# Kernel tuning notes

Hardware: AMD Instinct MI355X
Metric: run time of the kernel (lower is better)

The kernel has to match this reference:

```python
import jax, jax.numpy as jnp
import numpy as np

FDIM = 512
H = W = 64
D_STATE = 16
D_INNER = 2 * FDIM
DT_RANK = FDIM // 16
K = 4


def conv2d(x, w, b=None, padding=0, dilation=1, groups=1):
    out = jax.lax.conv_general_dilated(
        x, w, (1, 1), [(padding, padding), (padding, padding)],
        rhs_dilation=(dilation, dilation), feature_group_count=groups,
        dimension_numbers=('NCHW', 'OIHW', 'NCHW'))
    if b is not None:
        out = out + b[None, :, None, None]
    return out


def layernorm(x, g, b, axes):
    mu = jnp.mean(x, axes, keepdims=True)
    var = jnp.var(x, axes, keepdims=True)
    return (x - mu) * jax.lax.rsqrt(var + 1e-5) * g + b


def channel_shuffle(x, groups):
    B, C, Hh, Ww = x.shape
    return x.reshape(B, groups, C // groups, Hh, Ww).transpose(0, 2, 1, 3, 4).reshape(B, C, Hh, Ww)


def selective_scan(u, delta, A, Bs, Cs, D):
    # u, delta: (B,K,d,L); A: (K,d,N); Bs, Cs: (B,K,N,L); D: (K,d)
    Bsz, Kk, d, L = u.shape
    N = A.shape[-1]
    dT = jnp.moveaxis(delta, -1, 0)  # (L,B,K,d)
    uT = jnp.moveaxis(u, -1, 0)
    BT = jnp.moveaxis(Bs, -1, 0)     # (L,B,K,N)
    CT = jnp.moveaxis(Cs, -1, 0)

    @jax.checkpoint
    def step(hprev, inp):
        dt, ut, bt, ct = inp
        dA = jnp.exp(dt[..., None] * A)                       # (B,K,d,N)
        hnew = dA * hprev + (dt * ut)[..., None] * bt[:, :, None, :]
        yt = jnp.einsum('bkdn,bkn->bkd', hnew, ct)
        return hnew, yt

    h0 = jnp.zeros((Bsz, Kk, d, N), u.dtype)
    _, ys = jax.lax.scan(step, h0, (dT, uT, BT, CT))          # ys: (L,B,K,d)
    y = jnp.moveaxis(ys, 0, -1)                               # (B,K,d,L)
    return y + D[None, :, :, None] * u


def ss2d_core(x, x_proj_w, dt_w, dt_b, A_logs, Ds):
    # x: (B, d_inner, H, W) -> y: (B, d_inner, L), VMamba 4-direction cross-scan
    B, d, Hh, Ww = x.shape
    L = Hh * Ww
    xf = x.reshape(B, d, L)
    xwh = jnp.swapaxes(x, 2, 3).reshape(B, d, L)
    x_hwwh = jnp.stack([xf, xwh], axis=1)                     # (B,2,d,L)
    xs = jnp.concatenate([x_hwwh, jnp.flip(x_hwwh, axis=-1)], axis=1)  # (B,4,d,L)
    x_dbl = jnp.einsum('bkdl,kcd->bkcl', xs, x_proj_w)
    dts, Bs, Cs = jnp.split(x_dbl, [DT_RANK, DT_RANK + D_STATE], axis=2)
    dts = jnp.einsum('bkrl,kdr->bkdl', dts, dt_w)
    delta = jax.nn.softplus(dts + dt_b[None, :, :, None])
    A = -jnp.exp(A_logs)
    out_y = selective_scan(xs, delta, A, Bs, Cs, Ds)          # (B,4,d,L)
    inv_y = jnp.flip(out_y[:, 2:4], axis=-1)
    wh_y = jnp.swapaxes(out_y[:, 1].reshape(B, d, Ww, Hh), 2, 3).reshape(B, d, L)
    invwh_y = jnp.swapaxes(inv_y[:, 1].reshape(B, d, Ww, Hh), 2, 3).reshape(B, d, L)
    return out_y[:, 0] + inv_y[:, 0] + wh_y + invwh_y


def setup_inputs() -> dict:
    key = jax.random.key(0)
    ks = jax.random.split(key, 16)
    rn = lambda k, shape, s=0.02: jax.random.normal(k, shape, jnp.float32) * s
    inp = {
        'feature_embedding': jax.random.normal(ks[0], (1, FDIM, H, W), jnp.float32),
        'latent_embedding': jax.random.normal(ks[1], (1, FDIM, H, W), jnp.float32),
        'fg_w1': rn(ks[2], (FDIM // 16, 2 * FDIM, 1, 1)),
        'fg_b1': jnp.zeros((FDIM // 16,), jnp.float32),
        'fg_w2': rn(ks[3], (2 * FDIM, FDIM // 16, 1, 1)),
        'fg_b2': jnp.zeros((2 * FDIM,), jnp.float32),
        'fb_w1': rn(ks[4], (FDIM, 2 * FDIM, 3, 3)),
        'ln_g': jnp.ones((FDIM, H, W), jnp.float32),
        'ln_b': jnp.zeros((FDIM, H, W), jnp.float32),
        'fb_dw_w': rn(ks[5], (FDIM, 1, 3, 3), 0.1),
        'fb_dw_b': jnp.zeros((FDIM,), jnp.float32),
        'fb_pw1_w': rn(ks[6], (FDIM, FDIM, 1, 1)),
        'fb_pw1_b': jnp.zeros((FDIM,), jnp.float32),
        'fb_pw2_w': rn(ks[7], (FDIM, FDIM, 1, 1)),
        'fb_pw2_b': jnp.zeros((FDIM,), jnp.float32),
        'ln1_g': jnp.ones((FDIM,), jnp.float32),
        'ln1_b': jnp.zeros((FDIM,), jnp.float32),
        'in_proj_w': rn(ks[8], (2 * D_INNER, FDIM)),
        'dconv_w': rn(ks[9], (D_INNER, 1, 3, 3), 0.1),
        'dconv_b': jnp.zeros((D_INNER,), jnp.float32),
        'x_proj_w': rn(ks[10], (K, DT_RANK + 2 * D_STATE, D_INNER)),
        'dt_w': rn(ks[11], (K, D_INNER, DT_RANK), 0.1),
        'dt_b': rn(ks[12], (K, D_INNER), 0.1) - 4.0,
        'A_logs': jnp.broadcast_to(jnp.log(jnp.arange(1, D_STATE + 1, dtype=jnp.float32)), (K, D_INNER, D_STATE)) + 0.0,
        'Ds': jnp.ones((K, D_INNER), jnp.float32),
        'out_norm_g': jnp.ones((D_INNER,), jnp.float32),
        'out_norm_b': jnp.zeros((D_INNER,), jnp.float32),
        'out_proj_w': rn(ks[13], (FDIM, D_INNER)),
    }
    return inp


def reference(feature_embedding, latent_embedding, fg_w1, fg_b1, fg_w2, fg_b2,
              fb_w1, ln_g, ln_b, fb_dw_w, fb_dw_b, fb_pw1_w, fb_pw1_b,
              fb_pw2_w, fb_pw2_b, ln1_g, ln1_b, in_proj_w, dconv_w, dconv_b,
              x_proj_w, dt_w, dt_b, A_logs, Ds, out_norm_g, out_norm_b, out_proj_w):
    gelu = lambda v: jax.nn.gelu(v, approximate=False)
    concat = jnp.concatenate([feature_embedding, latent_embedding], axis=1)
    g = gelu(conv2d(concat, fg_w1, fg_b1))
    g = jax.nn.sigmoid(conv2d(g, fg_w2, fg_b2))
    wf = concat * g
    h = conv2d(wf, fb_w1, padding=1)
    h = gelu(layernorm(h, ln_g, ln_b, (1, 2, 3)))
    h = conv2d(h, fb_dw_w, fb_dw_b, padding=2, dilation=2, groups=FDIM)
    h = gelu(conv2d(h, fb_pw1_w, fb_pw1_b))
    h = channel_shuffle(h, 8)
    h = conv2d(h, fb_pw2_w, fb_pw2_b)
    fused = h + feature_embedding                              # (B,C,H,W)
    B = fused.shape[0]
    # VSSBlock: LN -> SS2D -> residual, operating on (B,H,W,C)
    x = jnp.transpose(fused, (0, 2, 3, 1))
    xn = layernorm(x, ln1_g, ln1_b, (3,))
    xz = xn @ in_proj_w.T                                      # (B,H,W,2*d_inner)
    xp, z = jnp.split(xz, 2, axis=-1)
    xc = jnp.transpose(xp, (0, 3, 1, 2))                       # (B,d_inner,H,W)
    xc = jax.nn.silu(conv2d(xc, dconv_w, dconv_b, padding=1, groups=D_INNER))
    y = ss2d_core(xc, x_proj_w, dt_w, dt_b, A_logs, Ds)        # (B,d_inner,L)
    y = jnp.transpose(y.reshape(B, D_INNER, H, W), (0, 2, 3, 1))
    y = layernorm(y, out_norm_g, out_norm_b, (3,))
    y = y * jax.nn.silu(z)
    attn = x + (y @ out_proj_w.T)                              # VSSBlock residual
    attn_out = jnp.transpose(attn, (0, 3, 1, 2))               # (B,C,H,W)
    blur_k = jnp.full((FDIM, 1, 3, 3), 1.0 / 9.0, attn_out.dtype)  # AvgPool2d(3,1,1)
    return conv2d(attn_out, blur_k, padding=1, groups=FDIM) + fused
```

## Files before the change

kernel.cpp:

```cpp
#include <hip/hip_runtime.h>


#define NT 4096
#define NCH 32
#define CHL 128

__device__ __forceinline__ float geluf(float x){ return 0.5f*x*(1.f+erff(x*0.70710678118654752f)); }
__device__ __forceinline__ float sigmf(float x){ return 1.f/(1.f+__expf(-x)); }
__device__ __forceinline__ float softplusf(float x){ return (x>20.f)? x : __logf(1.f+__expf(x)); }
__device__ __forceinline__ unsigned short f2b(float f){
  unsigned u = __float_as_uint(f);
  u += 0x7FFFu + ((u>>16)&1u);
  return (unsigned short)(u>>16);
}

template<int BMODE, int EPI, bool TRANSW, int ZB=0>
__launch_bounds__(256)
__global__ void k_gemm(int M, int K, int lda, int ldb,
    const float* __restrict__ A, const float* __restrict__ bias,
    const float* __restrict__ Bf, const float* __restrict__ Bc0,
    const float* __restrict__ Bc1, int rev, int shuf,
    const float* __restrict__ resf, float* __restrict__ out)
{
  __shared__ float smem[4352];
  float* As = smem;
  float* Bs = smem + 2176;
  const int t  = threadIdx.x;
  const int n0 = blockIdx.x*64, m0 = blockIdx.y*64;
  if (ZB==1){
    int z = blockIdx.z;
    A   += (size_t)z*64*1024;
    if (z&1) Bf = Bc0;
    rev  = (z>=2);
    out += (size_t)z*NT*64;
  } else if (ZB==2){
    int z = blockIdx.z;
    A    += (size_t)z*1024*32;
    bias += (size_t)z*1024;
    Bf   += (size_t)z*NT*64;
    out  += (size_t)z*1024*NT;
  }
  float acc[4][4] = {};

  for (int k0=0; k0<K; k0+=32){
    __syncthreads();
    {
      int m = t>>2, kk0 = (t&3)*8;
      float av[8] = {0,0,0,0,0,0,0,0};
      if (m0+m < M){
        const float* pa = A + (size_t)(m0+m)*lda + k0 + kk0;
        float4 a0 = *(const float4*)pa; float4 a1 = *(const float4*)(pa+4);
        av[0]=a0.x; av[1]=a0.y; av[2]=a0.z; av[3]=a0.w;
        av[4]=a1.x; av[5]=a1.y; av[6]=a1.z; av[7]=a1.w;
      }
      #pragma unroll
      for (int j=0;j<8;j++) As[(kk0+j)*68 + m] = av[j];
    }
    if (BMODE==2){
      int n = t>>2, kk0 = (t&3)*8;
      const float* p = Bf + (size_t)(n0+n)*ldb + k0 + kk0;
      float4 x0 = *(const float4*)p; float4 x1 = *(const float4*)(p+4);
      Bs[(kk0+0)*68+n]=x0.x; Bs[(kk0+1)*68+n]=x0.y; Bs[(kk0+2)*68+n]=x0.z; Bs[(kk0+3)*68+n]=x0.w;
      Bs[(kk0+4)*68+n]=x1.x; Bs[(kk0+5)*68+n]=x1.y; Bs[(kk0+6)*68+n]=x1.z; Bs[(kk0+7)*68+n]=x1.w;
    } else {
      int kk = t>>3, n8 = (t&7)*8;
      float bv[8];
      if (BMODE==0){
        int r = k0+kk; if (shuf) r = (r&7)*64 + (r>>3);
        const float* p = Bf + (size_t)r*NT;
        if (!rev){
          float4 x0 = *(const float4*)(p + n0+n8); float4 x1 = *(const float4*)(p + n0+n8+4);
          bv[0]=x0.x;bv[1]=x0.y;bv[2]=x0.z;bv[3]=x0.w;bv[4]=x1.x;bv[5]=x1.y;bv[6]=x1.z;bv[7]=x1.w;
        } else {
          const float* q = p + (4088 - n0 - n8);
          float4 x0 = *(const float4*)q; float4 x1 = *(const float4*)(q+4);
          bv[0]=x1.w;bv[1]=x1.z;bv[2]=x1.y;bv[3]=x1.x;bv[4]=x0.w;bv[5]=x0.z;bv[6]=x0.y;bv[7]=x0.x;
        }
      } else if (BMODE==1){
        int c = k0+kk;
        const float* p = (c<512) ? (Bc0 + (size_t)c*NT) : (Bc1 + (size_t)(c-512)*NT);
        float4 x0 = *(const float4*)(p + n0+n8); float4 x1 = *(const float4*)(p + n0+n8+4);
        bv[0]=x0.x;bv[1]=x0.y;bv[2]=x0.z;bv[3]=x0.w;bv[4]=x1.x;bv[5]=x1.y;bv[6]=x1.z;bv[7]=x1.w;
      } else {
        #pragma unroll
        for (int j=0;j<8;j++) bv[j] = 0.f;
      }
      *(float4*)&Bs[kk*68 + n8]   = make_float4(bv[0],bv[1],bv[2],bv[3]);
      *(float4*)&Bs[kk*68 + n8+4] = make_float4(bv[4],bv[5],bv[6],bv[7]);
    }
    __syncthreads();
    int ti = t>>4, tj = t&15;
    #pragma unroll
    for (int kk=0; kk<32; kk++){
      float4 a4 = *(const float4*)&As[kk*68 + ti*4];
      float4 b4 = *(const float4*)&Bs[kk*68 + tj*4];
      float aa[4] = {a4.x,a4.y,a4.z,a4.w};
      float bb[4] = {b4.x,b4.y,b4.z,b4.w};
      #pragma unroll
      for (int i=0;i<4;i++)
        #pragma unroll
        for (int j=0;j<4;j++) acc[i][j] += aa[i]*bb[j];
    }
  }

  int ti = t>>4, tj = t&15;
  if (!TRANSW){
    #pragma unroll
    for (int i=0;i<4;i++){
      int m = m0 + ti*4 + i;
      if (m >= M) continue;
      float bi = bias ? bias[m] : 0.f;
      float o4[4];
      #pragma unroll
      for (int j=0;j<4;j++){
        int n = n0 + tj*4 + j;
        float v = acc[i][j] + bi;
        if (EPI==1) v = geluf(v);
        else if (EPI==2) v = softplusf(v);
        else if (EPI==4) v = v + resf[(size_t)m*NT + n];
        else if (EPI==5){
          float cv = (m<512)? Bc0[(size_t)m*NT+n] : Bc1[(size_t)(m-512)*NT+n];
          v = cv * sigmf(v);
        }
        o4[j] = v;
      }
      *(float4*)&out[(size_t)m*NT + n0 + tj*4] = make_float4(o4[0],o4[1],o4[2],o4[3]);
    }
  } else {
    __syncthreads();
    #pragma unroll
    for (int i=0;i<4;i++)
      #pragma unroll
      for (int j=0;j<4;j++)
        smem[(tj*4+j)*68 + (ti*4+i)] = acc[i][j];
    __syncthreads();
    int nl = t>>2, c0 = (t&3)*16;
    #pragma unroll
    for (int g4=0; g4<4; g4++){
      float4 v = *(const float4*)&smem[nl*68 + c0 + g4*4];
      *(float4*)&out[(size_t)(n0+nl)*64 + c0 + g4*4] = v;
    }
  }
}

__global__ void k_cvt_bf16(const float* __restrict__ in, unsigned short* __restrict__ outp){
  size_t i = ((size_t)blockIdx.x*256 + threadIdx.x)*8;
  float4 a = *(const float4*)(in+i), b = *(const float4*)(in+i+4);
  unsigned short o[8] = { f2b(a.x),f2b(a.y),f2b(a.z),f2b(a.w),
                          f2b(b.x),f2b(b.y),f2b(b.z),f2b(b.w) };
  *(int4*)(outp+i) = *(int4*)o;
}

__global__ void k_cvt_wfrag(const float* __restrict__ w, int lda, int KSn,
                            unsigned short* __restrict__ outp){
  int tid = blockIdx.x*256 + threadIdx.x;
  int lane = tid & 63;
  int tmp = tid >> 6;
  int KS = tmp % KSn, MT = tmp / KSn;
  int m = MT*16 + (lane&15);
  int k = KS*32 + (lane>>4)*8;
  const float* p = w + (size_t)m*lda + k;
  float4 a = *(const float4*)p, b = *(const float4*)(p+4);
  unsigned short o[8] = { f2b(a.x),f2b(a.y),f2b(a.z),f2b(a.w),
                          f2b(b.x),f2b(b.y),f2b(b.z),f2b(b.w) };
  *(int4*)(outp + (size_t)tid*8) = *(int4*)o;
}

typedef __attribute__((ext_vector_type(8))) short bf16x8;
typedef __attribute__((ext_vector_type(4))) float f32x4;

__launch_bounds__(256)
__global__ void k_conv_mfma(const unsigned short* __restrict__ Wf,
                            const unsigned short* __restrict__ Bb,
                            float* __restrict__ outp){
  __shared__ unsigned short Bs[128*40];
  int t = threadIdx.x;
  int n0 = blockIdx.x*128, m0y = blockIdx.y;
  int kz = blockIdx.z;
  int w = t>>6, lane = t&63;
  int wm = (w>>1)*64, wn = (w&1)*64;
  int ln15 = lane&15, lhi = lane>>4;
  f32x4 acc[4][4] = {};
  int sn = t & 127, kh = t>>7;
  int p = n0 + sn, py = p>>6, px = p&63;

  for (int ks=0; ks<36; ks++){
    unsigned short tmp[16];
    int kbase = kz*1152 + ks*32 + kh*16;
    #pragma unroll
    for (int j=0;j<16;j++){
      int ka = kbase + j;
      int c = ka/9; int t9 = ka - c*9; int qy = t9/3;
      int dy = qy-1, dx = t9 - qy*3 - 1;
      int yy = py+dy, xx = px+dx;
      tmp[j] = (yy>=0 && yy<64 && xx>=0 && xx<64) ? Bb[(size_t)c*4096 + yy*64 + xx]
                                                  : (unsigned short)0;
    }
    __syncthreads();
    *(int4*)&Bs[sn*40 + kh*16]     = *(int4*)&tmp[0];
    *(int4*)&Bs[sn*40 + kh*16 + 8] = *(int4*)&tmp[8];
    __syncthreads();
    bf16x8 af[4], bf[4];
    int KSab = kz*36 + ks;
    #pragma unroll
    for (int fm=0; fm<4; fm++){
      int MT = m0y*8 + (w>>1)*4 + fm;
      af[fm] = *(const bf16x8*)&Wf[((size_t)MT*288 + KSab)*512 + lane*8];
    }
    #pragma unroll
    for (int fn=0; fn<4; fn++)
      bf[fn] = *(const bf16x8*)&Bs[(wn + fn*16 + ln15)*40 + lhi*8];
    #pragma unroll
    for (int fm=0; fm<4; fm++)
      #pragma unroll
      for (int fn=0; fn<4; fn++)
        acc[fm][fn] = __builtin_amdgcn_mfma_f32_16x16x32_bf16(af[fm], bf[fn], acc[fm][fn], 0,0,0);
  }
  float* op = outp + (size_t)kz*512*4096;
  #pragma unroll
  for (int fm=0; fm<4; fm++){
    #pragma unroll
    for (int fn=0; fn<4; fn++){
      int col = n0 + wn + fn*16 + ln15;
      int rowb = m0y*128 + wm + fm*16 + lhi*4;
      #pragma unroll
      for (int r=0; r<4; r++)
        op[(size_t)(rowb+r)*4096 + col] = acc[fm][fn][r];
    }
  }
}

template<int KSTEPS, int EPI>
__launch_bounds__(256)
__global__ void k_nhwc_mfma(const unsigned short* __restrict__ Wf,
                            const unsigned short* __restrict__ Bb, int ldb,
                            const float* __restrict__ resf,
                            float* __restrict__ outp){
  __shared__ unsigned short Bs[128*40];
  int t = threadIdx.x;
  int n0 = blockIdx.x*128, m0y = blockIdx.y;
  int w = t>>6, lane = t&63;
  int wm = (w>>1)*64, wn = (w&1)*64;
  int ln15 = lane&15, lhi = lane>>4;
  f32x4 acc[4][4] = {};
  int sn = t & 127, kh = t>>7;

  for (int ks=0; ks<KSTEPS; ks++){
    const unsigned short* src = Bb + (size_t)(n0+sn)*ldb + ks*32 + kh*16;
    int4 v0 = *(const int4*)src;
    int4 v1 = *(const int4*)(src+8);
    __syncthreads();
    *(int4*)&Bs[sn*40 + kh*16]     = v0;
    *(int4*)&Bs[sn*40 + kh*16 + 8] = v1;
    __syncthreads();
    bf16x8 af[4], bf[4];
    #pragma unroll
    for (int fm=0; fm<4; fm++){
      int MT = m0y*8 + (w>>1)*4 + fm;
      af[fm] = *(const bf16x8*)&Wf[((size_t)MT*KSTEPS + ks)*512 + lane*8];
    }
    #pragma unroll
    for (int fn=0; fn<4; fn++)
      bf[fn] = *(const bf16x8*)&Bs[(wn + fn*16 + ln15)*40 + lhi*8];
    #pragma unroll
    for (int fm=0; fm<4; fm++)
      #pragma unroll
      for (int fn=0; fn<4; fn++)
        acc[fm][fn] = __builtin_amdgcn_mfma_f32_16x16x32_bf16(af[fm], bf[fn], acc[fm][fn], 0,0,0);
  }
  #pragma unroll
  for (int fm=0; fm<4; fm++){
    #pragma unroll
    for (int fn=0; fn<4; fn++){
      int col = n0 + wn + fn*16 + ln15;
      int rowb = m0y*128 + wm + fm*16 + lhi*4;
      #pragma unroll
      for (int r=0; r<4; r++){
        float v = acc[fm][fn][r];
        if (EPI==4) v += resf[(size_t)(rowb+r)*4096 + col];
        outp[(size_t)(rowb+r)*4096 + col] = v;
      }
    }
  }
}

template<int DIL, int ACT>
__global__ void k_dwconv(const float* __restrict__ in, const float* __restrict__ w,
                         const float* __restrict__ b, float* __restrict__ out){
  int bid = blockIdx.x;
  int c = bid >> 4, yb = bid & 15;
  int t = threadIdx.x;
  int y = yb*4 + (t>>6), x = t&63;
  const float* pin = in + (size_t)c*NT;
  float acc = b[c];
  #pragma unroll
  for (int ky=0; ky<3; ky++){
    int yy = y + DIL*(ky-1);
    if (yy<0 || yy>=64) continue;
    #pragma unroll
    for (int kx=0; kx<3; kx++){
      int xx = x + DIL*(kx-1);
      if (xx<0 || xx>=64) continue;
      acc += w[c*9 + ky*3 + kx] * pin[yy*64+xx];
    }
  }
  if (ACT==1) acc = acc * sigmf(acc);
  out[(size_t)c*NT + y*64 + x] = acc;
}

__global__ void k_red_part8(const float* __restrict__ hp, float* __restrict__ h,
                            float* __restrict__ part){
  __shared__ float ls[256], lq[256];
  int t = threadIdx.x; size_t base = (size_t)blockIdx.x*4096 + t;
  const size_t SL = (size_t)512*4096;
  float s=0, q=0;
  #pragma unroll
  for (int i=0;i<16;i++){
    size_t idx = base + i*256;
    float v = 0.f;
    #pragma unroll
    for (int z=0; z<8; z++) v += hp[idx + z*SL];
    h[idx] = v; s+=v; q+=v*v;
  }
  ls[t]=s; lq[t]=q; __syncthreads();
  for (int off=128; off; off>>=1){ if (t<off){ ls[t]+=ls[t+off]; lq[t]+=lq[t+off]; } __syncthreads(); }
  if (t==0){ part[blockIdx.x] = ls[0]; part[512 + blockIdx.x] = lq[0]; }
}
__global__ void k_red_fin(const float* __restrict__ part, float* __restrict__ stats){
  __shared__ float ls[256], lq[256];
  int t = threadIdx.x;
  ls[t] = part[t] + part[t+256];
  lq[t] = part[512+t] + part[768+t];
  __syncthreads();
  for (int off=128; off; off>>=1){ if (t<off){ ls[t]+=ls[t+off]; lq[t]+=lq[t+off]; } __syncthreads(); }
  if (t==0){
    float mu = ls[0] * (1.f/2097152.f);
    float var = lq[0]*(1.f/2097152.f) - mu*mu;
    stats[0]=mu; stats[1]=rsqrtf(var + 1e-5f);
  }
}
__global__ void k_ln_gelu(const float* __restrict__ h, const float* __restrict__ g,
                          const float* __restrict__ b, const float* __restrict__ stats,
                          float* __restrict__ out){
  size_t idx = ((size_t)blockIdx.x*256 + threadIdx.x)*4;
  float mu = stats[0], rs = stats[1];
  float4 hv = *(const float4*)(h + idx);
  float4 gv = *(const float4*)(g + idx);
  float4 bv = *(const float4*)(b + idx);
  float4 o;
  o.x = geluf((hv.x-mu)*rs*gv.x+bv.x);
  o.y = geluf((hv.y-mu)*rs*gv.y+bv.y);
  o.z = geluf((hv.z-mu)*rs*gv.z+bv.z);
  o.w = geluf((hv.w-mu)*rs*gv.w+bv.w);
  *(float4*)(out + idx) = o;
}

__global__ void k_ln1_stats(const float* __restrict__ fused, float* __restrict__ mu1,
                            float* __restrict__ rs1){
  __shared__ float ss[256], sq[256];
  int t = threadIdx.x; int ci = t>>6; int pj = t&63;
  int pos = blockIdx.x*64 + pj;
  float s=0,q=0;
  for (int c=ci; c<512; c+=4){ float v = fused[(size_t)c*NT + pos]; s+=v; q+=v*v; }
  ss[t]=s; sq[t]=q; __syncthreads();
  if (ci==0){
    float S = ss[pj]+ss[64+pj]+ss[128+pj]+ss[192+pj];
    float Q = sq[pj]+sq[64+pj]+sq[128+pj]+sq[192+pj];
    float mu = S*(1.f/512.f);
    mu1[pos]=mu; rs1[pos]=rsqrtf(Q*(1.f/512.f) - mu*mu + 1e-5f);
  }
}
__global__ void k_ln1_apply(const float* __restrict__ fused, const float* __restrict__ g,
                            const float* __restrict__ b, const float* __restrict__ mu1,
                            const float* __restrict__ rs1, unsigned short* __restrict__ xnb){
  __shared__ float tile[64*65];
  int t = threadIdx.x;
  int p0 = blockIdx.x*64, c0 = blockIdx.y*64;
  for (int it=0; it<16; it++){
    int idx = t + it*256; int yy = idx>>6, xx = idx&63;
    tile[yy*65+xx] = fused[(size_t)(c0+yy)*NT + p0+xx];
  }
  __syncthreads();
  for (int it=0; it<16; it++){
    int idx = t + it*256; int r = idx>>6, s = idx&63;
    float v = tile[s*65+r];
    int pos = p0+r, c = c0+s;
    xnb[(size_t)pos*512 + c] = f2b((v - mu1[pos])*rs1[pos]*g[c] + b[c]);
  }
}

__global__ void k_transpose64(const float* __restrict__ in, float* __restrict__ out){
  __shared__ float tile[64*65];
  int d = blockIdx.x; int t = threadIdx.x;
  const float* p = in + (size_t)d*NT; float* q = out + (size_t)d*NT;
  for (int it=0; it<16; it++){
    int idx = t+it*256; int yy = idx>>6, xx = idx&63;
    tile[yy*65+xx] = p[idx];
  }
  __syncthreads();
  for (int it=0; it<16; it++){
    int idx = t+it*256; int w = idx>>6, hh = idx&63;
    q[idx] = tile[hh*65+w];
  }
}

__global__ void k_zero(float* __restrict__ p){
  size_t i = ((size_t)blockIdx.x*256 + threadIdx.x)*4;
  *(float4*)(p+i) = make_float4(0,0,0,0);
}

__launch_bounds__(256)
__global__ void k_scan_part(const float* __restrict__ delta, const float* __restrict__ xc,
                            const float* __restrict__ xcT, const float* __restrict__ xdblT,
                            const float* __restrict__ A_logs,
                            float* __restrict__ Pbuf, float* __restrict__ Sbuf){
  int bid = blockIdx.x;
  int c    = bid % NCH;
  int rest = bid / NCH;
  int k    = rest >> 4;
  int dblk = rest & 15;
  int w    = threadIdx.x >> 6;
  int lane = threadIdx.x & 63;
  int dsub = lane & 15, ngrp = lane >> 4;
  int d = dblk*64 + w*16 + dsub;
  const float* up = ((k&1)? xcT : xc) + (size_t)d*NT;
  const float* dp = delta + ((size_t)(k*1024 + d))*NT;
  const float* bc = xdblT + (size_t)k*NT*64;
  float A[4], S[4]={0,0,0,0}, P[4]={1.f,1.f,1.f,1.f};
  #pragma unroll
  for (int j=0;j<4;j++) A[j] = -__expf(A_logs[(size_t)(k*1024+d)*16 + ngrp*4 + j]);
  const bool rv = (k>=2);
  int base = c*CHL;
  for (int l0=base; l0<base+CHL; l0+=4){
    float4 dv4 = *(const float4*)(dp + l0);
    float4 uraw = rv ? *(const float4*)(up + (4092-l0)) : *(const float4*)(up + l0);
    float dts[4] = {dv4.x,dv4.y,dv4.z,dv4.w};
    float us[4];
    if (rv){ us[0]=uraw.w; us[1]=uraw.z; us[2]=uraw.y; us[3]=uraw.x; }
    else   { us[0]=uraw.x; us[1]=uraw.y; us[2]=uraw.z; us[3]=uraw.w; }
    #pragma unroll
    for (int s=0;s<4;s++){
      int l = l0+s;
      float dt = dts[s];
      float4 B4 = *(const float4*)(bc + (size_t)l*64 + 32 + ngrp*4);
      float xbu = dt*us[s];
      float Bv[4]={B4.x,B4.y,B4.z,B4.w};
      #pragma unroll
      for (int j=0;j<4;j++){
        float dA = __expf(dt*A[j]);
        S[j] = dA*S[j] + xbu*Bv[j];
        P[j] *= dA;
      }
    }
  }
  size_t o = ((size_t)(k*1024+d)*NCH + c)*16 + ngrp*4;
  *(float4*)&Pbuf[o] = make_float4(P[0],P[1],P[2],P[3]);
  *(float4*)&Sbuf[o] = make_float4(S[0],S[1],S[2],S[3]);
}

__global__ void k_scan_comb(const float* __restrict__ Pbuf, const float* __restrict__ Sbuf,
                            float* __restrict__ Hbuf){
  int tid = blockIdx.x*256 + threadIdx.x;
  int scan = tid >> 4, n = tid & 15;
  size_t base = (size_t)scan*(NCH*16) + n;
  float h = 0.f;
  #pragma unroll
  for (int c=0;c<NCH;c++){
    Hbuf[base + c*16] = h;
    h = Pbuf[base + c*16]*h + Sbuf[base + c*16];
  }
}

__launch_bounds__(256)
__global__ void k_scan_fin(const float* __restrict__ delta, const float* __restrict__ xc,
                           const float* __restrict__ xcT, const float* __restrict__ xdblT,
                           const float* __restrict__ A_logs, const float* __restrict__ Ds,
                           const float* __restrict__ Hbuf, float* __restrict__ ycomb){
  int bid = blockIdx.x;
  int c    = bid % NCH;
  int rest = bid / NCH;
  int k    = rest >> 4;
  int dblk = rest & 15;
  int w    = threadIdx.x >> 6;
  int lane = threadIdx.x & 63;
  int dsub = lane & 15, ngrp = lane >> 4;
  int d = dblk*64 + w*16 + dsub;
  const float* up = ((k&1)? xcT : xc) + (size_t)d*NT;
  const float* dp = delta + ((size_t)(k*1024 + d))*NT;
  const float* bc = xdblT + (size_t)k*NT*64;
  float A[4], h[4];
  #pragma unroll
  for (int j=0;j<4;j++) A[j] = -__expf(A_logs[(size_t)(k*1024+d)*16 + ngrp*4 + j]);
  {
    size_t o = ((size_t)(k*1024+d)*NCH + c)*16 + ngrp*4;
    float4 h4 = *(const float4*)&Hbuf[o];
    h[0]=h4.x; h[1]=h4.y; h[2]=h4.z; h[3]=h4.w;
  }
  float Dv = Ds[k*1024+d];
  const bool rv = (k>=2);
  int base = c*CHL;
  for (int l0=base; l0<base+CHL; l0+=4){
    float4 dv4 = *(const float4*)(dp + l0);
    float4 uraw = rv ? *(const float4*)(up + (4092-l0)) : *(const float4*)(up + l0);
    float dts[4] = {dv4.x,dv4.y,dv4.z,dv4.w};
    float us[4];
    if (rv){ us[0]=uraw.w; us[1]=uraw.z; us[2]=uraw.y; us[3]=uraw.x; }
    else   { us[0]=uraw.x; us[1]=uraw.y; us[2]=uraw.z; us[3]=uraw.w; }
    #pragma unroll
    for (int s=0;s<4;s++){
      int l = l0+s;
      float dt = dts[s], u = us[s];
      float4 B4 = *(const float4*)(bc + (size_t)l*64 + 32 + ngrp*4);
      float4 C4 = *(const float4*)(bc + (size_t)l*64 + 48 + ngrp*4);
      float xbu = dt*u;
      float Bv[4]={B4.x,B4.y,B4.z,B4.w}, Cv[4]={C4.x,C4.y,C4.z,C4.w};
      float ys = 0.f;
      #pragma unroll
      for (int j=0;j<4;j++){
        float dA = __expf(dt*A[j]);
        h[j] = dA*h[j] + xbu*Bv[j];
        ys += h[j]*Cv[j];
      }
      ys += __shfl_xor(ys, 16);
      ys += __shfl_xor(ys, 32);
      if (ngrp==0){
        int pos;
        if (k==0) pos = l;
        else if (k==1) pos = ((l&63)<<6) | (l>>6);
        else if (k==2) pos = 4095-l;
        else { int tt = 4095-l; pos = ((tt&63)<<6) | (tt>>6); }
        atomicAdd(&ycomb[(size_t)pos*1024 + d], ys + Dv*u);
      }
    }
  }
}

__global__ void k_combine(const float* __restrict__ ycomb, const float* __restrict__ xz,
                          const float* __restrict__ g, const float* __restrict__ b,
                          unsigned short* __restrict__ yactb){
  int pos = blockIdx.x, t = threadIdx.x;
  float v[4]; float s=0,q=0;
  #pragma unroll
  for (int i=0;i<4;i++){ v[i] = ycomb[(size_t)pos*1024 + t + i*256]; s+=v[i]; q+=v[i]*v[i]; }
  #pragma unroll
  for (int off=32; off>=1; off>>=1){ s += __shfl_xor(s,off); q += __shfl_xor(q,off); }
  __shared__ float red[8];
  int wid = t>>6;
  if ((t&63)==0){ red[wid*2]=s; red[wid*2+1]=q; }
  __syncthreads();
  float S = red[0]+red[2]+red[4]+red[6];
  float Q = red[1]+red[3]+red[5]+red[7];
  float mu = S*(1.f/1024.f), rs = rsqrtf(Q*(1.f/1024.f) - mu*mu + 1e-5f);
  #pragma unroll
  for (int i=0;i<4;i++){
    int dd = t + i*256;
    float z = xz[(size_t)(1024+dd)*NT + pos];
    float yv = (v[i]-mu)*rs*g[dd] + b[dd];
    yactb[(size_t)pos*1024 + dd] = f2b(yv * (z * sigmf(z)));
  }
}

__global__ void k_blur(const float* __restrict__ attn, const float* __restrict__ fused,
                       float* __restrict__ outp){
  int bid = blockIdx.x; int c = bid>>4, yb = bid&15; int t = threadIdx.x;
  int y = yb*4 + (t>>6), x = t&63;
  const float* p = attn + (size_t)c*NT;
  float s = 0;
  #pragma unroll
  for (int dy=-1; dy<=1; dy++){
    int yy = y+dy; if (yy<0||yy>=64) continue;
    #pragma unroll
    for (int dx=-1; dx<=1; dx++){
      int xx = x+dx; if (xx<0||xx>=64) continue;
      s += p[yy*64+xx];
    }
  }
  float val = s*(1.f/9.f) + fused[(size_t)c*NT + y*64 + x];
  outp[(size_t)c*NT + y*64 + x] = val;
}

extern "C" void kernel_launch(void* const* d_in, const int* in_sizes, int n_in,
                              void* d_out, int out_size, void* d_ws, size_t ws_size,
                              hipStream_t stream){
  const float* feat = (const float*)d_in[0];
  const float* lat  = (const float*)d_in[1];
  const float* fg_w1= (const float*)d_in[2];
  const float* fg_b1= (const float*)d_in[3];
  const float* fg_w2= (const float*)d_in[4];
  const float* fg_b2= (const float*)d_in[5];
  const float* fb_w1= (const float*)d_in[6];
  const float* ln_g = (const float*)d_in[7];
  const float* ln_b = (const float*)d_in[8];
  const float* dw_w = (const float*)d_in[9];
  const float* dw_b = (const float*)d_in[10];
  const float* pw1_w= (const float*)d_in[11];
  const float* pw1_b= (const float*)d_in[12];
  const float* pw2_w= (const float*)d_in[13];
  const float* pw2_b= (const float*)d_in[14];
  const float* ln1_g= (const float*)d_in[15];
  const float* ln1_b= (const float*)d_in[16];
  const float* inpw = (const float*)d_in[17];
  const float* dc_w = (const float*)d_in[18];
  const float* dc_b = (const float*)d_in[19];
  const float* xpw  = (const float*)d_in[20];
  const float* dtw  = (const float*)d_in[21];
  const float* dtb  = (const float*)d_in[22];
  const float* Alog = (const float*)d_in[23];
  const float* Dsp  = (const float*)d_in[24];
  const float* ong  = (const float*)d_in[25];
  const float* onb  = (const float*)d_in[26];
  const float* opw  = (const float*)d_in[27];
  float* outp = (float*)d_out;
  (void)in_sizes; (void)n_in; (void)out_size; (void)ws_size;

  float* Wp = (float*)d_ws;
  size_t off = 0;
  auto alloc = [&](size_t n){ float* p = Wp + off; off += n; return p; };
  float* S0    = alloc((size_t)1024*NT);
  float* S1    = alloc((size_t)512*NT);
  float* P0    = alloc((size_t)512*NT);
  float* P1    = alloc((size_t)2048*NT);
  float* P2    = alloc((size_t)1024*NT);
  float* P3    = alloc((size_t)1024*NT);
  float* P4    = alloc((size_t)4*NT*64);
  float* P5    = alloc((size_t)4*1024*NT);
  float* P6    = alloc((size_t)1024*NT);
  float* part  = alloc(1024);
  float* stats = alloc(4);
  float* mu1   = alloc(4096);
  float* rs1   = alloc(4096);

  float* wf    = S0;
  float* h     = S1;
  float* h2    = P1;
  float* h3    = S1;
  float* h4    = P2;
  float* fused = P0;
  float* xz    = P1;
  float* xc    = P2;
  float* xcT   = P3;
  float* xdblT = P4;
  float* hpart = P5;
  float* delta = P5;
  float* g1    = P6;
  float* ycomb = P6;
  float* attn  = S1;
  unsigned short* wf_bf   = (unsigned short*)(P1 + (size_t)512*NT);
  unsigned short* w_frag  = (unsigned short*)(P1 + (size_t)1024*NT);
  unsigned short* xnb     = (unsigned short*)S0;
  unsigned short* w_frag2 = (unsigned short*)P5;
  unsigned short* yactb   = (unsigned short*)S0;
  unsigned short* w_frag3 = (unsigned short*)P5;
  float* Pbuf  = S0;
  float* Sbuf  = S0 + (size_t)2*1048576;
  float* Hbuf  = S1;

  hipLaunchKernelGGL((k_gemm<1,1,false>), dim3(64,1), dim3(256), 0, stream,
      32, 1024, 1024, 0, fg_w1, fg_b1, nullptr, feat, lat, 0,0, nullptr, g1);
  hipLaunchKernelGGL((k_gemm<0,5,false>), dim3(64,16), dim3(256), 0, stream,
      1024, 32, 32, 0, fg_w2, fg_b2, g1, feat, lat, 0,0, nullptr, wf);
  hipLaunchKernelGGL(k_cvt_bf16, dim3(2048), dim3(256), 0, stream, wf, wf_bf);
  hipLaunchKernelGGL(k_cvt_wfrag, dim3(2304), dim3(256), 0, stream, fb_w1, 9216, 288, w_frag);
  hipLaunchKernelGGL(k_conv_mfma, dim3(32,4,8), dim3(256), 0, stream, w_frag, wf_bf, hpart);
  hipLaunchKernelGGL(k_red_part8, dim3(512), dim3(256), 0, stream, hpart, h, part);
  hipLaunchKernelGGL(k_red_fin,  dim3(1),   dim3(256), 0, stream, part, stats);
  hipLaunchKernelGGL(k_ln_gelu,  dim3(2048),dim3(256), 0, stream, h, ln_g, ln_b, stats, h2);
  hipLaunchKernelGGL((k_dwconv<2,0>), dim3(512*16), dim3(256), 0, stream, h2, dw_w, dw_b, h3);
  hipLaunchKernelGGL((k_gemm<0,1,false>), dim3(64,8), dim3(256), 0, stream,
      512, 512, 512, 0, pw1_w, pw1_b, h3, nullptr,nullptr, 0,0, nullptr, h4);
  hipLaunchKernelGGL((k_gemm<0,4,false>), dim3(64,8), dim3(256), 0, stream,
      512, 512, 512, 0, pw2_w, pw2_b, h4, nullptr,nullptr, 0,1, feat, fused);
  hipLaunchKernelGGL(k_ln1_stats, dim3(64), dim3(256), 0, stream, fused, mu1, rs1);
  hipLaunchKernelGGL(k_ln1_apply, dim3(64,8), dim3(256), 0, stream, fused, ln1_g, ln1_b, mu1, rs1, xnb);
  hipLaunchKernelGGL(k_cvt_wfrag, dim3(512), dim3(256), 0, stream, inpw, 512, 16, w_frag2);
  hipLaunchKernelGGL((k_nhwc_mfma<16,0>), dim3(32,16), dim3(256), 0, stream,
      w_frag2, xnb, 512, nullptr, xz);
  hipLaunchKernelGGL((k_dwconv<1,1>), dim3(1024*16), dim3(256), 0, stream, xz, dc_w, dc_b, xc);
  hipLaunchKernelGGL(k_transpose64, dim3(1024), dim3(256), 0, stream, xc, xcT);
  hipLaunchKernelGGL((k_gemm<0,0,true,1>), dim3(64,1,4), dim3(256), 0, stream,
      64, 1024, 1024, 0, xpw, nullptr, xc, xcT, nullptr, 0,0, nullptr, xdblT);
  hipLaunchKernelGGL((k_gemm<2,2,false,2>), dim3(64,16,4), dim3(256), 0, stream,
      1024, 32, 32, 64, dtw, dtb, xdblT, nullptr,nullptr, 0,0, nullptr, delta);
  hipLaunchKernelGGL(k_zero, dim3(4096), dim3(256), 0, stream, ycomb);
  hipLaunchKernelGGL(k_scan_part, dim3(64*NCH), dim3(256), 0, stream,
      delta, xc, xcT, xdblT, Alog, Pbuf, Sbuf);
  hipLaunchKernelGGL(k_scan_comb, dim3(256), dim3(256), 0, stream, Pbuf, Sbuf, Hbuf);
  hipLaunchKernelGGL(k_scan_fin, dim3(64*NCH), dim3(256), 0, stream,
      delta, xc, xcT, xdblT, Alog, Dsp, Hbuf, ycomb);
  hipLaunchKernelGGL(k_combine, dim3(4096), dim3(256), 0, stream, ycomb, xz, ong, onb, yactb);
  hipLaunchKernelGGL(k_cvt_wfrag, dim3(256), dim3(256), 0, stream, opw, 1024, 32, w_frag3);
  hipLaunchKernelGGL((k_nhwc_mfma<32,4>), dim3(32,4), dim3(256), 0, stream,
      w_frag3, yactb, 1024, fused, attn);
  hipLaunchKernelGGL(k_blur, dim3(512*16), dim3(256), 0, stream, attn, fused, outp);
}
```

Before: 1.052 ms.

## Move pointwise convs to bf16 MFMA GEMM and stage scan inputs in LDS

The two 512x512 pointwise convolutions in the feature block now run on the bf16 MFMA NHWC GEMM kernel instead of the fp32 generic GEMM. A new transpose-and-convert kernel produces bf16 NHWC activations, and the channel shuffle is folded into its index mapping. The MFMA kernel gains bias and GELU epilogues. Separately, both selective-scan kernels stage delta and u for 32-step chunks in shared memory with coalesced loads, replacing the per-thread strided row reads. The cost is extra conversion passes and lower precision in the pointwise convolutions.

```diff
diff --git a/kernel.cpp b/kernel.cpp
--- a/kernel.cpp
+++ b/kernel.cpp
@@ -151,6 +151,23 @@
   *(int4*)(outp+i) = *(int4*)o;
 }
 
+__global__ void k_cvtT_bf16(const float* __restrict__ in, int shuf,
+                            unsigned short* __restrict__ outp){
+  __shared__ float tile[64*65];
+  int t = threadIdx.x;
+  int p0 = blockIdx.x*64, c0 = blockIdx.y*64;
+  for (int it=0; it<16; it++){
+    int idx = t + it*256; int yy = idx>>6, xx = idx&63;
+    int c = c0 + yy; int src = shuf ? (c&7)*64 + (c>>3) : c;
+    tile[yy*65+xx] = in[(size_t)src*NT + p0+xx];
+  }
+  __syncthreads();
+  for (int it=0; it<16; it++){
+    int idx = t + it*256; int r = idx>>6, s = idx&63;
+    outp[(size_t)(p0+r)*512 + c0+s] = f2b(tile[s*65+r]);
+  }
+}
+
 __global__ void k_cvt_wfrag(const float* __restrict__ w, int lda, int KSn,
                             unsigned short* __restrict__ outp){
   int tid = blockIdx.x*256 + threadIdx.x;
@@ -234,6 +251,7 @@
 __launch_bounds__(256)
 __global__ void k_nhwc_mfma(const unsigned short* __restrict__ Wf,
                             const unsigned short* __restrict__ Bb, int ldb,
+                            const float* __restrict__ bias,
                             const float* __restrict__ resf,
                             float* __restrict__ outp){
   __shared__ unsigned short Bs[128*40];
@@ -276,9 +294,11 @@
       int rowb = m0y*128 + wm + fm*16 + lhi*4;
       #pragma unroll
       for (int r=0; r<4; r++){
-        float v = acc[fm][fn][r];
-        if (EPI==4) v += resf[(size_t)(rowb+r)*4096 + col];
-        outp[(size_t)(rowb+r)*4096 + col] = v;
+        int m = rowb + r;
+        float v = acc[fm][fn][r] + (bias ? bias[m] : 0.f);
+        if (EPI==1) v = geluf(v);
+        else if (EPI==4) v += resf[(size_t)m*4096 + col];
+        outp[(size_t)m*4096 + col] = v;
       }
     }
   }
@@ -414,36 +434,47 @@
                             const float* __restrict__ xcT, const float* __restrict__ xdblT,
                             const float* __restrict__ A_logs,
                             float* __restrict__ Pbuf, float* __restrict__ Sbuf){
+  __shared__ float dtile[64*36], utile[64*36];
   int bid = blockIdx.x;
   int c    = bid % NCH;
   int rest = bid / NCH;
   int k    = rest >> 4;
   int dblk = rest & 15;
-  int w    = threadIdx.x >> 6;
-  int lane = threadIdx.x & 63;
+  int t = threadIdx.x;
+  int w = t>>6, lane = t&63;
   int dsub = lane & 15, ngrp = lane >> 4;
-  int d = dblk*64 + w*16 + dsub;
-  const float* up = ((k&1)? xcT : xc) + (size_t)d*NT;
-  const float* dp = delta + ((size_t)(k*1024 + d))*NT;
+  int dd = w*16 + dsub;
+  int d = dblk*64 + dd;
+  int ld_dd = t>>2, q = t&3;
+  const bool rv = (k>=2);
+  const float* dprow = delta + ((size_t)(k*1024 + dblk*64 + ld_dd))*NT;
+  const float* uprow = ((k&1)? xcT : xc) + (size_t)(dblk*64 + ld_dd)*NT;
   const float* bc = xdblT + (size_t)k*NT*64;
   float A[4], S[4]={0,0,0,0}, P[4]={1.f,1.f,1.f,1.f};
   #pragma unroll
   for (int j=0;j<4;j++) A[j] = -__expf(A_logs[(size_t)(k*1024+d)*16 + ngrp*4 + j]);
-  const bool rv = (k>=2);
   int base = c*CHL;
-  for (int l0=base; l0<base+CHL; l0+=4){
-    float4 dv4 = *(const float4*)(dp + l0);
-    float4 uraw = rv ? *(const float4*)(up + (4092-l0)) : *(const float4*)(up + l0);
-    float dts[4] = {dv4.x,dv4.y,dv4.z,dv4.w};
-    float us[4];
-    if (rv){ us[0]=uraw.w; us[1]=uraw.z; us[2]=uraw.y; us[3]=uraw.x; }
-    else   { us[0]=uraw.x; us[1]=uraw.y; us[2]=uraw.z; us[3]=uraw.w; }
-    #pragma unroll
-    for (int s=0;s<4;s++){
-      int l = l0+s;
-      float dt = dts[s];
+  for (int l0=0; l0<CHL; l0+=32){
+    int L0 = base + l0;
+    __syncthreads();
+    {
+      const float* dp8 = dprow + L0 + q*8;
+      float4 a0 = *(const float4*)dp8, a1 = *(const float4*)(dp8+4);
+      *(float4*)&dtile[ld_dd*36 + q*8]     = a0;
+      *(float4*)&dtile[ld_dd*36 + q*8 + 4] = a1;
+      int us = rv ? (4064 - L0) : L0;
+      const float* up8 = uprow + us + q*8;
+      float4 b0 = *(const float4*)up8, b1 = *(const float4*)(up8+4);
+      *(float4*)&utile[ld_dd*36 + q*8]     = b0;
+      *(float4*)&utile[ld_dd*36 + q*8 + 4] = b1;
+    }
+    __syncthreads();
+    for (int s=0; s<32; s++){
+      int l = L0 + s;
+      float dt = dtile[dd*36 + s];
+      float u  = utile[dd*36 + (rv ? 31-s : s)];
       float4 B4 = *(const float4*)(bc + (size_t)l*64 + 32 + ngrp*4);
-      float xbu = dt*us[s];
+      float xbu = dt*u;
       float Bv[4]={B4.x,B4.y,B4.z,B4.w};
       #pragma unroll
       for (int j=0;j<4;j++){
@@ -476,17 +507,21 @@
                            const float* __restrict__ xcT, const float* __restrict__ xdblT,
                            const float* __restrict__ A_logs, const float* __restrict__ Ds,
                            const float* __restrict__ Hbuf, float* __restrict__ ycomb){
+  __shared__ float dtile[64*36], utile[64*36];
   int bid = blockIdx.x;
   int c    = bid % NCH;
   int rest = bid / NCH;
   int k    = rest >> 4;
   int dblk = rest & 15;
-  int w    = threadIdx.x >> 6;
-  int lane = threadIdx.x & 63;
+  int t = threadIdx.x;
+  int w = t>>6, lane = t&63;
   int dsub = lane & 15, ngrp = lane >> 4;
-  int d = dblk*64 + w*16 + dsub;
-  const float* up = ((k&1)? xcT : xc) + (size_t)d*NT;
-  const float* dp = delta + ((size_t)(k*1024 + d))*NT;
+  int dd = w*16 + dsub;
+  int d = dblk*64 + dd;
+  int ld_dd = t>>2, q = t&3;
+  const bool rv = (k>=2);
+  const float* dprow = delta + ((size_t)(k*1024 + dblk*64 + ld_dd))*NT;
+  const float* uprow = ((k&1)? xcT : xc) + (size_t)(dblk*64 + ld_dd)*NT;
   const float* bc = xdblT + (size_t)k*NT*64;
   float A[4], h[4];
   #pragma unroll
@@ -497,19 +532,26 @@
     h[0]=h4.x; h[1]=h4.y; h[2]=h4.z; h[3]=h4.w;
   }
   float Dv = Ds[k*1024+d];
-  const bool rv = (k>=2);
   int base = c*CHL;
-  for (int l0=base; l0<base+CHL; l0+=4){
-    float4 dv4 = *(const float4*)(dp + l0);
-    float4 uraw = rv ? *(const float4*)(up + (4092-l0)) : *(const float4*)(up + l0);
-    float dts[4] = {dv4.x,dv4.y,dv4.z,dv4.w};
-    float us[4];
-    if (rv){ us[0]=uraw.w; us[1]=uraw.z; us[2]=uraw.y; us[3]=uraw.x; }
-    else   { us[0]=uraw.x; us[1]=uraw.y; us[2]=uraw.z; us[3]=uraw.w; }
-    #pragma unroll
-    for (int s=0;s<4;s++){
-      int l = l0+s;
-      float dt = dts[s], u = us[s];
+  for (int l0=0; l0<CHL; l0+=32){
+    int L0 = base + l0;
+    __syncthreads();
+    {
+      const float* dp8 = dprow + L0 + q*8;
+      float4 a0 = *(const float4*)dp8, a1 = *(const float4*)(dp8+4);
+      *(float4*)&dtile[ld_dd*36 + q*8]     = a0;
+      *(float4*)&dtile[ld_dd*36 + q*8 + 4] = a1;
+      int us = rv ? (4064 - L0) : L0;
+      const float* up8 = uprow + us + q*8;
+      float4 b0 = *(const float4*)up8, b1 = *(const float4*)(up8+4);
+      *(float4*)&utile[ld_dd*36 + q*8]     = b0;
+      *(float4*)&utile[ld_dd*36 + q*8 + 4] = b1;
+    }
+    __syncthreads();
+    for (int s=0; s<32; s++){
+      int l = L0 + s;
+      float dt = dtile[dd*36 + s];
+      float u  = utile[dd*36 + (rv ? 31-s : s)];
       float4 B4 = *(const float4*)(bc + (size_t)l*64 + 32 + ngrp*4);
       float4 C4 = *(const float4*)(bc + (size_t)l*64 + 48 + ngrp*4);
       float xbu = dt*u;
@@ -651,6 +693,10 @@
   unsigned short* w_frag2 = (unsigned short*)P5;
   unsigned short* yactb   = (unsigned short*)S0;
   unsigned short* w_frag3 = (unsigned short*)P5;
+  unsigned short* wfpw1   = (unsigned short*)P5;
+  unsigned short* wfpw2   = (unsigned short*)(P5 + (size_t)131072);
+  unsigned short* h3T     = (unsigned short*)(P5 + (size_t)1048576);
+  unsigned short* h4T     = (unsigned short*)(P5 + (size_t)2097152);
   float* Pbuf  = S0;
   float* Sbuf  = S0 + (size_t)2*1048576;
   float* Hbuf  = S1;
@@ -666,15 +712,19 @@
   hipLaunchKernelGGL(k_red_fin,  dim3(1),   dim3(256), 0, stream, part, stats);
   hipLaunchKernelGGL(k_ln_gelu,  dim3(2048),dim3(256), 0, stream, h, ln_g, ln_b, stats, h2);
   hipLaunchKernelGGL((k_dwconv<2,0>), dim3(512*16), dim3(256), 0, stream, h2, dw_w, dw_b, h3);
-  hipLaunchKernelGGL((k_gemm<0,1,false>), dim3(64,8), dim3(256), 0, stream,
-      512, 512, 512, 0, pw1_w, pw1_b, h3, nullptr,nullptr, 0,0, nullptr, h4);
-  hipLaunchKernelGGL((k_gemm<0,4,false>), dim3(64,8), dim3(256), 0, stream,
-      512, 512, 512, 0, pw2_w, pw2_b, h4, nullptr,nullptr, 0,1, feat, fused);
+  hipLaunchKernelGGL(k_cvtT_bf16, dim3(64,8), dim3(256), 0, stream, h3, 0, h3T);
+  hipLaunchKernelGGL(k_cvt_wfrag, dim3(128), dim3(256), 0, stream, pw1_w, 512, 16, wfpw1);
+  hipLaunchKernelGGL((k_nhwc_mfma<16,1>), dim3(32,4), dim3(256), 0, stream,
+      wfpw1, h3T, 512, pw1_b, nullptr, h4);
+  hipLaunchKernelGGL(k_cvtT_bf16, dim3(64,8), dim3(256), 0, stream, h4, 1, h4T);
+  hipLaunchKernelGGL(k_cvt_wfrag, dim3(128), dim3(256), 0, stream, pw2_w, 512, 16, wfpw2);
+  hipLaunchKernelGGL((k_nhwc_mfma<16,4>), dim3(32,4), dim3(256), 0, stream,
+      wfpw2, h4T, 512, pw2_b, feat, fused);
   hipLaunchKernelGGL(k_ln1_stats, dim3(64), dim3(256), 0, stream, fused, mu1, rs1);
   hipLaunchKernelGGL(k_ln1_apply, dim3(64,8), dim3(256), 0, stream, fused, ln1_g, ln1_b, mu1, rs1, xnb);
   hipLaunchKernelGGL(k_cvt_wfrag, dim3(512), dim3(256), 0, stream, inpw, 512, 16, w_frag2);
   hipLaunchKernelGGL((k_nhwc_mfma<16,0>), dim3(32,16), dim3(256), 0, stream,
-      w_frag2, xnb, 512, nullptr, xz);
+      w_frag2, xnb, 512, nullptr, nullptr, xz);
   hipLaunchKernelGGL((k_dwconv<1,1>), dim3(1024*16), dim3(256), 0, stream, xz, dc_w, dc_b, xc);
   hipLaunchKernelGGL(k_transpose64, dim3(1024), dim3(256), 0, stream, xc, xcT);
   hipLaunchKernelGGL((k_gemm<0,0,true,1>), dim3(64,1,4), dim3(256), 0, stream,
@@ -690,6 +740,6 @@
   hipLaunchKernelGGL(k_combine, dim3(4096), dim3(256), 0, stream, ycomb, xz, ong, onb, yactb);
   hipLaunchKernelGGL(k_cvt_wfrag, dim3(256), dim3(256), 0, stream, opw, 1024, 32, w_frag3);
   hipLaunchKernelGGL((k_nhwc_mfma<32,4>), dim3(32,4), dim3(256), 0, stream,
-      w_frag3, yactb, 1024, fused, attn);
+      w_frag3, yactb, 1024, nullptr, fused, attn);
   hipLaunchKernelGGL(k_blur, dim3(512*16), dim3(256), 0, stream, attn, fused, outp);
 }
```

Result: faster. 942.3 us (-10.4%).
